# Optimization experiments

Measured on AMD Instinct MI355X. Metric: run time of the kernel, lower is better.

The kernel has to match this reference:

```python
import jax, jax.numpy as jnp
import numpy as np

V, D, H, F = 50257, 180, 18, 720
S = 2048
DK = D // H  # 10
EPS = 1e-5


def _layernorm(x, g, b):
    mu = jnp.mean(x, axis=-1, keepdims=True)
    var = jnp.mean(jnp.square(x - mu), axis=-1, keepdims=True)
    return (x - mu) * jax.lax.rsqrt(var + EPS) * g + b


def _pos_encoding(seq_len, d_model):
    pos = jnp.arange(seq_len, dtype=jnp.float32)[:, None]            # [S,1]
    i = jnp.arange(d_model // 2, dtype=jnp.float32)[None, :]         # [1,D/2]
    angle = pos / jnp.power(10000.0, 2.0 * i / d_model)              # [S,D/2]
    pe = jnp.zeros((seq_len, d_model), dtype=jnp.float32)
    pe = pe.at[:, 0::2].set(jnp.sin(angle))
    pe = pe.at[:, 1::2].set(jnp.cos(angle))
    return pe


def setup_inputs() -> dict:
    key = jax.random.key(0)
    ks = jax.random.split(key, 16)

    def xavier(k, shape):
        fan_out, fan_in = shape[0], shape[-1]
        lim = float(np.sqrt(6.0 / (fan_in + fan_out)))
        return jax.random.uniform(k, shape, jnp.float32, -lim, lim)

    return {
        "input_ids": jax.random.randint(ks[0], (S,), 0, V),
        "emb": xavier(ks[1], (V, D)),
        "Wq": xavier(ks[2], (D, D)),
        "Wk": xavier(ks[3], (D, D)),
        "Wv": xavier(ks[4], (D, D)),
        "g1": jnp.ones((D,), jnp.float32),
        "beta1": jnp.zeros((D,), jnp.float32),
        "W1": xavier(ks[5], (F, D)),
        "bf1": jnp.zeros((F,), jnp.float32),
        "W2": xavier(ks[6], (D, F)),
        "bf2": jnp.zeros((D,), jnp.float32),
        "g2": jnp.ones((D,), jnp.float32),
        "beta2": jnp.zeros((D,), jnp.float32),
        "Wo": xavier(ks[7], (V, D)),
        "bo": jnp.zeros((V,), jnp.float32),
    }


def reference(input_ids, emb, Wq, Wk, Wv, g1, beta1, W1, bf1, W2, bf2, g2, beta2, Wo, bo):
    seq_len = input_ids.shape[0]
    x = emb[input_ids] + _pos_encoding(seq_len, D)                   # [S,D]

    # QKV projections (no bias), split into heads: [H,S,DK]
    q = (x @ Wq.T).reshape(seq_len, H, DK).transpose(1, 0, 2)
    k = (x @ Wk.T).reshape(seq_len, H, DK).transpose(1, 0, 2)
    v = (x @ Wv.T).reshape(seq_len, H, DK).transpose(1, 0, 2)

    scores = jnp.einsum("hqd,hkd->hqk", q, k) / jnp.sqrt(jnp.float32(DK))
    causal = jnp.tril(jnp.ones((seq_len, seq_len), dtype=bool))
    scores = jnp.where(causal[None, :, :], scores, -1e9)
    attn = jax.nn.softmax(scores, axis=-1)
    out = jnp.einsum("hqk,hkd->hqd", attn, v)                        # [H,S,DK]
    attn_out = out.transpose(1, 0, 2).reshape(seq_len, D)

    x = _layernorm(x + attn_out, g1, beta1)
    ff = jax.nn.gelu(x @ W1.T + bf1, approximate=False) @ W2.T + bf2
    x = _layernorm(x + ff, g2, beta2)

    logits = x @ Wo.T + bo                                           # [S,V]
    return logits
```

## Files before the change

### kernel.cpp

```cpp
#include <hip/hip_runtime.h>
#include <hip/hip_bf16.h>

#define S 2048
#define D 180
#define H 18
#define DKH 10
#define F 720
#define V 50257
#define VP 51200
#define KP 192
#define EPS 1e-5f
#define NEGINF (-1e30f)

typedef __attribute__((ext_vector_type(8))) short bf16x8;
typedef __attribute__((ext_vector_type(4))) float f32x4;

__global__ void k_wbconv(const float* __restrict__ Wo, __hip_bfloat16* __restrict__ wb) {
    int idx = blockIdx.x * 256 + threadIdx.x;
    const int total = VP * 24;
    if (idx >= total) return;
    int n = idx / 24;
    int k0 = (idx - n * 24) * 8;
    __hip_bfloat16 tmp[8];
    #pragma unroll
    for (int j = 0; j < 8; ++j) {
        int k = k0 + j;
        float v = (n < V && k < D) ? Wo[n * D + k] : 0.0f;
        tmp[j] = __float2bfloat16(v);
    }
    *(bf16x8*)((short*)wb + n * KP + k0) = *(bf16x8*)tmp;
}

__global__ void k_transposeAll(const float* __restrict__ Wq, const float* __restrict__ Wk,
                               const float* __restrict__ Wv, const float* __restrict__ W1,
                               const float* __restrict__ W2,
                               float* __restrict__ WqT, float* __restrict__ WkT,
                               float* __restrict__ WvT, float* __restrict__ W1T,
                               float* __restrict__ W2T) {
    __shared__ float tile[32][33];
    const float* src; float* dst; int R, C;
    switch (blockIdx.y) {
        case 0: src = Wq; dst = WqT; R = D; C = D; break;
        case 1: src = Wk; dst = WkT; R = D; C = D; break;
        case 2: src = Wv; dst = WvT; R = D; C = D; break;
        case 3: src = W1; dst = W1T; R = F; C = D; break;
        default: src = W2; dst = W2T; R = D; C = F; break;
    }
    int tilesC = (C + 31) >> 5;
    int tr = (blockIdx.x / tilesC) * 32, tc = (blockIdx.x % tilesC) * 32;
    if (tr >= R) return;
    int lx = threadIdx.x & 31, ly = threadIdx.x >> 5;
    #pragma unroll
    for (int rr = ly; rr < 32; rr += 8) {
        int r = tr + rr, c = tc + lx;
        tile[rr][lx] = (r < R && c < C) ? src[r * C + c] : 0.0f;
    }
    __syncthreads();
    #pragma unroll
    for (int rr = ly; rr < 32; rr += 8) {
        int c = tc + rr, r = tr + lx;
        if (c < C && r < R) dst[c * R + r] = tile[lx][rr];
    }
}

__global__ void k_qkv(const int* __restrict__ ids, const float* __restrict__ emb,
                      const float* __restrict__ WqT, const float* __restrict__ WkT,
                      const float* __restrict__ WvT,
                      float* __restrict__ x0, float* __restrict__ qkv) {
    const int R = 8;
    __shared__ float xs[R * D];
    int r0 = blockIdx.x * R;
    const float* WT = (blockIdx.y == 0) ? WqT : ((blockIdx.y == 1) ? WkT : WvT);
    float* out = qkv + blockIdx.y * (S * D);
    for (int idx = threadIdx.x; idx < R * D; idx += 192) {
        int r = idx / D, d = idx - r * D;
        int row = r0 + r;
        int i = d >> 1;
        float inv = exp2f(-0.14764124866166054f * (float)i);
        float ang = (float)row * inv;
        float pe = (d & 1) ? cosf(ang) : sinf(ang);
        float v = emb[(size_t)ids[row] * D + d] + pe;
        xs[idx] = v;
        if (blockIdx.y == 0) x0[(size_t)row * D + d] = v;
    }
    __syncthreads();
    int d = threadIdx.x;
    if (d < D) {
        float acc[R] = {};
        for (int k0 = 0; k0 < D; k0 += 4) {
            f32x4 xr[R];
            #pragma unroll
            for (int r = 0; r < R; ++r) xr[r] = *(const f32x4*)&xs[r * D + k0];
            #pragma unroll
            for (int j = 0; j < 4; ++j) {
                float wv = WT[(k0 + j) * D + d];
                #pragma unroll
                for (int r = 0; r < R; ++r) acc[r] += xr[r][j] * wv;
            }
        }
        #pragma unroll
        for (int r = 0; r < R; ++r) out[(r0 + r) * D + d] = acc[r];
    }
}

__global__ __launch_bounds__(256) void k_attn1(const float* __restrict__ qkv,
                                               float* __restrict__ part) {
    int c = blockIdx.x, qt = blockIdx.y, h = blockIdx.z;
    if (4 * c > qt) return;
    __shared__ float Ks[256][12];
    __shared__ float Vs[256][12];
    __shared__ float cmb[4][64][13];
    int j0 = c * 256, q0 = qt * 64;
    int t = threadIdx.x;
    int lane = t & 63, w = t >> 6;
    const float* kp = qkv + S * D + h * DKH;
    const float* vp = qkv + 2 * S * D + h * DKH;
    for (int e = t; e < 256 * DKH; e += 256) {
        int jj = e / DKH, cc = e - jj * DKH;
        Ks[jj][cc] = kp[(j0 + jj) * D + cc];
        Vs[jj][cc] = vp[(j0 + jj) * D + cc];
    }
    __syncthreads();
    int qi = q0 + lane;
    float qv[DKH];
    #pragma unroll
    for (int cc = 0; cc < DKH; ++cc) qv[cc] = qkv[qi * D + h * DKH + cc];
    float m = NEGINF, l = 0.0f, acc[DKH] = {};
    const float scale = 0.31622776601683794f;
    #pragma unroll
    for (int blk = 0; blk < 8; ++blk) {
        float sv[8], tm = NEGINF;
        #pragma unroll
        for (int u = 0; u < 8; ++u) {
            int jj = w * 64 + blk * 8 + u;
            int j = j0 + jj;
            f32x4 k0 = *(const f32x4*)&Ks[jj][0];
            f32x4 k1 = *(const f32x4*)&Ks[jj][4];
            f32x4 k2 = *(const f32x4*)&Ks[jj][8];
            float s = qv[0]*k0[0] + qv[1]*k0[1] + qv[2]*k0[2] + qv[3]*k0[3]
                    + qv[4]*k1[0] + qv[5]*k1[1] + qv[6]*k1[2] + qv[7]*k1[3]
                    + qv[8]*k2[0] + qv[9]*k2[1];
            sv[u] = (j <= qi) ? s * scale : NEGINF;
            tm = fmaxf(tm, sv[u]);
        }
        float nm = fmaxf(m, tm);
        if (nm > -0.5e30f) {
            float cor = __expf(m - nm);
            l *= cor;
            #pragma unroll
            for (int cc = 0; cc < DKH; ++cc) acc[cc] *= cor;
            m = nm;
            #pragma unroll
            for (int u = 0; u < 8; ++u) {
                float p = __expf(sv[u] - m);
                int jj = w * 64 + blk * 8 + u;
                l += p;
                f32x4 v0 = *(const f32x4*)&Vs[jj][0];
                f32x4 v1 = *(const f32x4*)&Vs[jj][4];
                f32x4 v2 = *(const f32x4*)&Vs[jj][8];
                acc[0] += p * v0[0]; acc[1] += p * v0[1];
                acc[2] += p * v0[2]; acc[3] += p * v0[3];
                acc[4] += p * v1[0]; acc[5] += p * v1[1];
                acc[6] += p * v1[2]; acc[7] += p * v1[3];
                acc[8] += p * v2[0]; acc[9] += p * v2[1];
            }
        }
    }
    cmb[w][lane][0] = m;
    cmb[w][lane][1] = l;
    #pragma unroll
    for (int cc = 0; cc < DKH; ++cc) cmb[w][lane][2 + cc] = acc[cc];
    __syncthreads();
    if (t < 64) {
        float M = NEGINF;
        #pragma unroll
        for (int ww = 0; ww < 4; ++ww) M = fmaxf(M, cmb[ww][t][0]);
        float L = 0.0f, o[DKH] = {};
        #pragma unroll
        for (int ww = 0; ww < 4; ++ww) {
            float e = __expf(cmb[ww][t][0] - M);
            L += e * cmb[ww][t][1];
            #pragma unroll
            for (int cc = 0; cc < DKH; ++cc) o[cc] += e * cmb[ww][t][2 + cc];
        }
        float* pp = part + (((size_t)(h * 32 + qt) * 9 + c) * 64 + t) * 12;
        pp[0] = M; pp[1] = L;
        #pragma unroll
        for (int cc = 0; cc < DKH; ++cc) pp[2 + cc] = o[cc];
    }
}

__global__ void k_attn2(const float* __restrict__ part, float* __restrict__ ao) {
    int qt = blockIdx.x, h = blockIdx.y;
    int q = threadIdx.x;
    int nch = qt / 4 + 1;
    float m = NEGINF, l = 0.0f, acc[DKH] = {};
    for (int c = 0; c < nch; ++c) {
        const float* pp = part + (((size_t)(h * 32 + qt) * 9 + c) * 64 + q) * 12;
        float pm = pp[0], pl = pp[1];
        float nm = fmaxf(m, pm);
        float c1 = __expf(m - nm), c2 = __expf(pm - nm);
        l = l * c1 + pl * c2;
        #pragma unroll
        for (int cc = 0; cc < DKH; ++cc)
            acc[cc] = acc[cc] * c1 + pp[2 + cc] * c2;
        m = nm;
    }
    float inv = 1.0f / l;
    float* op = ao + (size_t)(qt * 64 + q) * D + h * DKH;
    #pragma unroll
    for (int cc = 0; cc < DKH; ++cc) op[cc] = acc[cc] * inv;
}

__device__ inline float wave_sum(float v) {
    #pragma unroll
    for (int o = 32; o > 0; o >>= 1) v += __shfl_xor(v, o);
    return v;
}

__global__ void k_ln1(const float* __restrict__ x0, const float* __restrict__ ao,
                      const float* __restrict__ g, const float* __restrict__ b,
                      float* __restrict__ x1) {
    int row = blockIdx.x * 4 + (threadIdx.x >> 6);
    int lane = threadIdx.x & 63;
    const float* pa = x0 + row * D;
    const float* pb = ao + row * D;
    float v[3];
    int c[3];
    float sum = 0.0f;
    #pragma unroll
    for (int k = 0; k < 3; ++k) {
        c[k] = lane + 64 * k;
        v[k] = (c[k] < D) ? (pa[c[k]] + pb[c[k]]) : 0.0f;
        sum += v[k];
    }
    sum = wave_sum(sum);
    float mu = sum / (float)D;
    float ss = 0.0f;
    #pragma unroll
    for (int k = 0; k < 3; ++k) {
        float dd = (c[k] < D) ? (v[k] - mu) : 0.0f;
        ss += dd * dd;
    }
    ss = wave_sum(ss);
    float rs = rsqrtf(ss / (float)D + EPS);
    #pragma unroll
    for (int k = 0; k < 3; ++k)
        if (c[k] < D) x1[row * D + c[k]] = (v[k] - mu) * rs * g[c[k]] + b[c[k]];
}

__global__ __launch_bounds__(768) void k_ffn(const float* __restrict__ x1,
                     const float* __restrict__ W1T, const float* __restrict__ bf1,
                     const float* __restrict__ W2T, const float* __restrict__ bf2,
                     const float* __restrict__ g, const float* __restrict__ b,
                     __hip_bfloat16* __restrict__ xb) {
    const int R = 8;
    __shared__ float xs[R * D];
    __shared__ float ys[R * F];
    __shared__ float red[2][4][3][2];
    int r0 = blockIdx.x * R;
    int t = threadIdx.x;
    for (int idx = t; idx < R * D / 4; idx += 768)
        *(f32x4*)&xs[idx * 4] = *(const f32x4*)&x1[(size_t)r0 * D + idx * 4];
    __syncthreads();
    if (t < F) {
        float acc[R] = {};
        for (int k0 = 0; k0 < D; k0 += 4) {
            f32x4 xr[R];
            #pragma unroll
            for (int r = 0; r < R; ++r) xr[r] = *(const f32x4*)&xs[r * D + k0];
            #pragma unroll
            for (int j = 0; j < 4; ++j) {
                float wv = W1T[(k0 + j) * F + t];
                #pragma unroll
                for (int r = 0; r < R; ++r) acc[r] += xr[r][j] * wv;
            }
        }
        float bb = bf1[t];
        #pragma unroll
        for (int r = 0; r < R; ++r) {
            float vv = acc[r] + bb;
            ys[r * F + t] = 0.5f * vv * (1.0f + erff(vv * 0.7071067811865475f));
        }
    }
    __syncthreads();
    int gq = t / 192;
    int d = t - gq * 192;
    int wig = d >> 6;
    int lane = d & 63;
    int row0 = gq * 2, row1 = gq * 2 + 1;
    float v0 = 0.0f, v1 = 0.0f;
    if (d < D) {
        float a0 = 0.0f, a1 = 0.0f;
        for (int k0 = 0; k0 < F; k0 += 4) {
            f32x4 ya = *(const f32x4*)&ys[row0 * F + k0];
            f32x4 yb = *(const f32x4*)&ys[row1 * F + k0];
            #pragma unroll
            for (int j = 0; j < 4; ++j) {
                float wv = W2T[(k0 + j) * D + d];
                a0 += ya[j] * wv;
                a1 += yb[j] * wv;
            }
        }
        float bb = bf2[d];
        v0 = x1[(size_t)(r0 + row0) * D + d] + a0 + bb;
        v1 = x1[(size_t)(r0 + row1) * D + d] + a1 + bb;
    }
    {
        float s1 = wave_sum(v0), q1 = wave_sum(v0 * v0);
        float s2 = wave_sum(v1), q2 = wave_sum(v1 * v1);
        if (lane == 0) {
            red[0][gq][wig][0] = s1; red[1][gq][wig][0] = q1;
            red[0][gq][wig][1] = s2; red[1][gq][wig][1] = q2;
        }
    }
    __syncthreads();
    float sum0 = red[0][gq][0][0] + red[0][gq][1][0] + red[0][gq][2][0];
    float sq0  = red[1][gq][0][0] + red[1][gq][1][0] + red[1][gq][2][0];
    float sum1 = red[0][gq][0][1] + red[0][gq][1][1] + red[0][gq][2][1];
    float sq1  = red[1][gq][0][1] + red[1][gq][1][1] + red[1][gq][2][1];
    float mu0 = sum0 / (float)D, var0 = sq0 / (float)D - mu0 * mu0;
    float mu1 = sum1 / (float)D, var1 = sq1 / (float)D - mu1 * mu1;
    float rs0 = rsqrtf(var0 + EPS), rs1 = rsqrtf(var1 + EPS);
    float gd = (d < D) ? g[d] : 0.0f, bd = (d < D) ? b[d] : 0.0f;
    float o0 = (d < D) ? ((v0 - mu0) * rs0 * gd + bd) : 0.0f;
    float o1 = (d < D) ? ((v1 - mu1) * rs1 * gd + bd) : 0.0f;
    xb[(size_t)(r0 + row0) * KP + d] = __float2bfloat16(o0);
    xb[(size_t)(r0 + row1) * KP + d] = __float2bfloat16(o1);
}

__global__ __launch_bounds__(1024) void k_logits(const __hip_bfloat16* __restrict__ xbp,
                         const __hip_bfloat16* __restrict__ wbp,
                         const float* __restrict__ bo, float* __restrict__ out) {
    __shared__ float stg[16][16][68];
    int Lb = blockIdx.x;
    int wg = (Lb & 7) * 200 + (Lb >> 3);
    int mblk = wg & 31;
    int pblk = wg >> 5;
    int m0 = mblk * 64, n0 = pblk * 1024;
    int t = threadIdx.x;
    int lane = t & 63, wid = t >> 6;
    int r16 = lane & 15, kg = lane >> 4;
    int colbase = n0 + wid * 64;
    const short* xs = (const short*)xbp;
    const short* ws = (const short*)wbp;
    f32x4 acc[4][4] = {};
    int mrow[4], nrow[4];
    #pragma unroll
    for (int mi = 0; mi < 4; ++mi) mrow[mi] = m0 + mi * 16 + r16;
    #pragma unroll
    for (int ni = 0; ni < 4; ++ni) nrow[ni] = colbase + ni * 16 + r16;
    bf16x8 a0[4], b0[4];
    #pragma unroll
    for (int mi = 0; mi < 4; ++mi) a0[mi] = *(const bf16x8*)(xs + mrow[mi] * KP + kg * 8);
    #pragma unroll
    for (int ni = 0; ni < 4; ++ni) b0[ni] = *(const bf16x8*)(ws + nrow[ni] * KP + kg * 8);
    #pragma unroll
    for (int kk = 0; kk < 6; ++kk) {
        bf16x8 a1[4], b1[4];
        if (kk < 5) {
            int kb = (kk + 1) * 32 + kg * 8;
            #pragma unroll
            for (int mi = 0; mi < 4; ++mi) a1[mi] = *(const bf16x8*)(xs + mrow[mi] * KP + kb);
            #pragma unroll
            for (int ni = 0; ni < 4; ++ni) b1[ni] = *(const bf16x8*)(ws + nrow[ni] * KP + kb);
        }
        #pragma unroll
        for (int mi = 0; mi < 4; ++mi)
            #pragma unroll
            for (int ni = 0; ni < 4; ++ni)
                acc[mi][ni] = __builtin_amdgcn_mfma_f32_16x16x32_bf16(b0[ni], a0[mi], acc[mi][ni], 0, 0, 0);
        if (kk < 5) {
            #pragma unroll
            for (int mi = 0; mi < 4; ++mi) a0[mi] = a1[mi];
            #pragma unroll
            for (int ni = 0; ni < 4; ++ni) b0[ni] = b1[ni];
        }
    }
    bool ok = (colbase + lane < V);
    #pragma unroll
    for (int mi = 0; mi < 4; ++mi) {
        #pragma unroll
        for (int ni = 0; ni < 4; ++ni) {
            int cn = colbase + ni * 16 + kg * 4;
            f32x4 r = acc[mi][ni];
            if (cn + 3 < V) {
                f32x4 bv = *(const f32x4*)(bo + cn);
                r += bv;
            } else {
                #pragma unroll
                for (int j = 0; j < 4; ++j) r[j] += (cn + j < V) ? bo[cn + j] : 0.0f;
            }
            *(f32x4*)&stg[wid][r16][ni * 16 + kg * 4] = r;
        }
        float vals[16];
        #pragma unroll
        for (int rr = 0; rr < 16; ++rr) vals[rr] = stg[wid][rr][lane];
        float* p = out + (size_t)(m0 + mi * 16) * V + colbase + lane;
        #pragma unroll
        for (int rr = 0; rr < 16; ++rr) {
            if (ok) *p = vals[rr];
            p += V;
        }
    }
}

extern "C" void kernel_launch(void* const* d_in, const int* in_sizes, int n_in,
                              void* d_out, int out_size, void* d_ws, size_t ws_size,
                              hipStream_t stream) {
    const int* ids   = (const int*)d_in[0];
    const float* emb = (const float*)d_in[1];
    const float* Wq  = (const float*)d_in[2];
    const float* Wk  = (const float*)d_in[3];
    const float* Wv  = (const float*)d_in[4];
    const float* g1  = (const float*)d_in[5];
    const float* b1  = (const float*)d_in[6];
    const float* W1  = (const float*)d_in[7];
    const float* bf1 = (const float*)d_in[8];
    const float* W2  = (const float*)d_in[9];
    const float* bf2 = (const float*)d_in[10];
    const float* g2  = (const float*)d_in[11];
    const float* b2  = (const float*)d_in[12];
    const float* Wo  = (const float*)d_in[13];
    const float* bo  = (const float*)d_in[14];
    float* out = (float*)d_out;

    char* w = (char*)d_ws;
    float* x0 = (float*)w;           w += S * D * 4;
    float* qkv = (float*)w;          w += 3 * S * D * 4;
    float* ao = (float*)w;           w += S * D * 4;
    float* x1 = (float*)w;           w += S * D * 4;
    float* WqT = (float*)w;          w += D * D * 4;
    float* WkT = (float*)w;          w += D * D * 4;
    float* WvT = (float*)w;          w += D * D * 4;
    float* W1T = (float*)w;          w += F * D * 4;
    float* W2T = (float*)w;          w += D * F * 4;
    float* part = (float*)w;         w += (size_t)H * 32 * 9 * 64 * 12 * 4;
    __hip_bfloat16* xb = (__hip_bfloat16*)w; w += S * KP * 2;
    __hip_bfloat16* wb = (__hip_bfloat16*)w; w += (size_t)VP * KP * 2;

    k_wbconv<<<dim3((VP * 24 + 255) / 256), 256, 0, stream>>>(Wo, wb);
    k_transposeAll<<<dim3(138, 5), 256, 0, stream>>>(Wq, Wk, Wv, W1, W2,
                                                     WqT, WkT, WvT, W1T, W2T);
    k_qkv<<<dim3(S / 8, 3), 192, 0, stream>>>(ids, emb, WqT, WkT, WvT, x0, qkv);
    k_attn1<<<dim3(9, 32, H), 256, 0, stream>>>(qkv, part);
    k_attn2<<<dim3(32, H), 64, 0, stream>>>(part, ao);
    k_ln1<<<dim3(S / 4), 256, 0, stream>>>(x0, ao, g1, b1, x1);
    k_ffn<<<dim3(S / 8), 768, 0, stream>>>(x1, W1T, bf1, W2T, bf2, g2, b2, xb);
    k_logits<<<dim3(1600), 1024, 0, stream>>>(xb, wb, bo, out);
}
```

Baseline: 413.8 us.

## Split logits GEMM into tiled bf16 store plus separate relayout pass

The logits GEMM now writes bias-added results as bf16 into a tile-contiguous workspace buffer instead of staging them through shared memory into the strided fp32 output. A separate grid-stride kernel then reads those tiles and expands them to fp32 rows of the final output. The aim is to drop the LDS staging and make the GEMM's stores contiguous. The cost is an extra intermediate write and read, plus logits rounded to bf16 precision. The old direct kernel is kept as a fallback when the workspace is too small.

```diff
diff --git a/kernel.cpp b/kernel.cpp
--- a/kernel.cpp
+++ b/kernel.cpp
@@ -13,6 +13,7 @@
 #define NEGINF (-1e30f)
 
 typedef __attribute__((ext_vector_type(8))) short bf16x8;
+typedef __attribute__((ext_vector_type(4))) short short4v;
 typedef __attribute__((ext_vector_type(4))) float f32x4;
 
 __global__ void k_wbconv(const float* __restrict__ Wo, __hip_bfloat16* __restrict__ wb) {
@@ -329,7 +330,101 @@
     xb[(size_t)(r0 + row1) * KP + d] = __float2bfloat16(o1);
 }
 
-__global__ __launch_bounds__(1024) void k_logits(const __hip_bfloat16* __restrict__ xbp,
+__global__ __launch_bounds__(1024) void k_logits_g(const __hip_bfloat16* __restrict__ xbp,
+                         const __hip_bfloat16* __restrict__ wbp,
+                         const float* __restrict__ bo, short* __restrict__ lgt) {
+    int Lb = blockIdx.x;
+    int wg = (Lb & 7) * 200 + (Lb >> 3);
+    int mblk = wg & 31;
+    int pblk = wg >> 5;
+    int m0 = mblk * 64, n0 = pblk * 1024;
+    int t = threadIdx.x;
+    int lane = t & 63, wid = t >> 6;
+    int r16 = lane & 15, kg = lane >> 4;
+    int colbase = n0 + wid * 64;
+    const short* xs = (const short*)xbp;
+    const short* ws = (const short*)wbp;
+    f32x4 acc[4][4] = {};
+    int mrow[4], nrow[4];
+    #pragma unroll
+    for (int mi = 0; mi < 4; ++mi) mrow[mi] = m0 + mi * 16 + r16;
+    #pragma unroll
+    for (int ni = 0; ni < 4; ++ni) nrow[ni] = colbase + ni * 16 + r16;
+    bf16x8 a0[4], b0[4];
+    #pragma unroll
+    for (int mi = 0; mi < 4; ++mi) a0[mi] = *(const bf16x8*)(xs + mrow[mi] * KP + kg * 8);
+    #pragma unroll
+    for (int ni = 0; ni < 4; ++ni) b0[ni] = *(const bf16x8*)(ws + nrow[ni] * KP + kg * 8);
+    #pragma unroll
+    for (int kk = 0; kk < 6; ++kk) {
+        bf16x8 a1[4], b1[4];
+        if (kk < 5) {
+            int kb = (kk + 1) * 32 + kg * 8;
+            #pragma unroll
+            for (int mi = 0; mi < 4; ++mi) a1[mi] = *(const bf16x8*)(xs + mrow[mi] * KP + kb);
+            #pragma unroll
+            for (int ni = 0; ni < 4; ++ni) b1[ni] = *(const bf16x8*)(ws + nrow[ni] * KP + kb);
+        }
+        #pragma unroll
+        for (int mi = 0; mi < 4; ++mi)
+            #pragma unroll
+            for (int ni = 0; ni < 4; ++ni)
+                acc[mi][ni] = __builtin_amdgcn_mfma_f32_16x16x32_bf16(b0[ni], a0[mi], acc[mi][ni], 0, 0, 0);
+        if (kk < 5) {
+            #pragma unroll
+            for (int mi = 0; mi < 4; ++mi) a0[mi] = a1[mi];
+            #pragma unroll
+            for (int ni = 0; ni < 4; ++ni) b0[ni] = b1[ni];
+        }
+    }
+    short* dst = lgt + ((size_t)(mblk * 50 + pblk) << 16);
+    #pragma unroll
+    for (int mi = 0; mi < 4; ++mi) {
+        #pragma unroll
+        for (int ni = 0; ni < 4; ++ni) {
+            int cn = colbase + ni * 16 + kg * 4;
+            f32x4 r = acc[mi][ni];
+            if (cn + 3 < V) {
+                f32x4 bv = *(const f32x4*)(bo + cn);
+                r += bv;
+            } else {
+                #pragma unroll
+                for (int j = 0; j < 4; ++j) r[j] += (cn + j < V) ? bo[cn + j] : 0.0f;
+            }
+            short4v h;
+            #pragma unroll
+            for (int j = 0; j < 4; ++j)
+                h[j] = (short)__hip_bfloat16_raw(__float2bfloat16(r[j])).x;
+            int off = (mi * 16 + r16) * 1024 + wid * 64 + ni * 16 + kg * 4;
+            *(short4v*)(dst + off) = h;
+        }
+    }
+}
+
+#define C4PR 12565
+__global__ void k_relayout(const short* __restrict__ lgt, float* __restrict__ out) {
+    const unsigned total = (unsigned)S * C4PR;
+    for (unsigned w = blockIdx.x * 256 + threadIdx.x; w < total; w += gridDim.x * 256) {
+        unsigned row = w / C4PR;
+        unsigned c4 = w - row * C4PR;
+        unsigned col = c4 * 4;
+        unsigned tc = col >> 10, wc = col & 1023;
+        const short* p = lgt + (((size_t)((row >> 6) * 50 + tc)) << 16)
+                       + (row & 63) * 1024 + wc;
+        short4v h = *(const short4v*)p;
+        float* po = out + (size_t)row * V + col;
+        int n = V - col; n = (n > 4) ? 4 : n;
+        #pragma unroll
+        for (int j = 0; j < 4; ++j) {
+            if (j < n) {
+                unsigned u = ((unsigned)(unsigned short)h[j]) << 16;
+                po[j] = __uint_as_float(u);
+            }
+        }
+    }
+}
+
+__global__ __launch_bounds__(1024) void k_logits_direct(const __hip_bfloat16* __restrict__ xbp,
                          const __hip_bfloat16* __restrict__ wbp,
                          const float* __restrict__ bo, float* __restrict__ out) {
     __shared__ float stg[16][16][68];
@@ -438,6 +533,8 @@
     float* part = (float*)w;         w += (size_t)H * 32 * 9 * 64 * 12 * 4;
     __hip_bfloat16* xb = (__hip_bfloat16*)w; w += S * KP * 2;
     __hip_bfloat16* wb = (__hip_bfloat16*)w; w += (size_t)VP * KP * 2;
+    short* lgt = (short*)w;
+    size_t need = (size_t)(w - (char*)d_ws) + (size_t)S * VP * 2;
 
     k_wbconv<<<dim3((VP * 24 + 255) / 256), 256, 0, stream>>>(Wo, wb);
     k_transposeAll<<<dim3(138, 5), 256, 0, stream>>>(Wq, Wk, Wv, W1, W2,
@@ -447,5 +544,10 @@
     k_attn2<<<dim3(32, H), 64, 0, stream>>>(part, ao);
     k_ln1<<<dim3(S / 4), 256, 0, stream>>>(x0, ao, g1, b1, x1);
     k_ffn<<<dim3(S / 8), 768, 0, stream>>>(x1, W1T, bf1, W2T, bf2, g2, b2, xb);
-    k_logits<<<dim3(1600), 1024, 0, stream>>>(xb, wb, bo, out);
-}
+    if (ws_size >= need) {
+        k_logits_g<<<dim3(1600), 1024, 0, stream>>>(xb, wb, bo, lgt);
+        k_relayout<<<dim3(2048), 256, 0, stream>>>(lgt, out);
+    } else {
+        k_logits_direct<<<dim3(1600), 1024, 0, stream>>>(xb, wb, bo, out);
+    }
+}
```

Result: slower. 611.2 us (+47.7%).

## Restructure logits GEMM into LDS-staged 128x128 tiles with 2x2 wave layout

Applied to the files above, without the earlier changes.

Replaces the logits kernel, which read A and B fragments directly from global memory with 1024-thread blocks, with a 256-thread, 128x128-tile kernel. Each block stages A and B chunks of 64 K-elements into padded shared memory, prefetching the next chunk into registers while computing on the current one. The aim is to cut redundant global reads through reuse inside shared memory. The output epilogue now writes four scalar floats per lane directly instead of transposing through shared memory. That drops the coalesced store path for the 400MB output and may make the store-bound part worse.

```diff
diff --git a/kernel.cpp b/kernel.cpp
--- a/kernel.cpp
+++ b/kernel.cpp
@@ -11,6 +11,7 @@
 #define KP 192
 #define EPS 1e-5f
 #define NEGINF (-1e30f)
+#define LSTR 72
 
 typedef __attribute__((ext_vector_type(8))) short bf16x8;
 typedef __attribute__((ext_vector_type(4))) float f32x4;
@@ -329,80 +330,110 @@
     xb[(size_t)(r0 + row1) * KP + d] = __float2bfloat16(o1);
 }
 
-__global__ __launch_bounds__(1024) void k_logits(const __hip_bfloat16* __restrict__ xbp,
+__global__ __launch_bounds__(256) void k_logits(const __hip_bfloat16* __restrict__ xbp,
                          const __hip_bfloat16* __restrict__ wbp,
                          const float* __restrict__ bo, float* __restrict__ out) {
-    __shared__ float stg[16][16][68];
+    __shared__ short As[128 * LSTR];
+    __shared__ short Bs[128 * LSTR];
     int Lb = blockIdx.x;
-    int wg = (Lb & 7) * 200 + (Lb >> 3);
-    int mblk = wg & 31;
-    int pblk = wg >> 5;
-    int m0 = mblk * 64, n0 = pblk * 1024;
+    int wg = (Lb & 7) * 800 + (Lb >> 3);
+    int mblk = wg & 15;
+    int pblk = wg >> 4;
+    int m0 = mblk * 128, n0 = pblk * 128;
     int t = threadIdx.x;
     int lane = t & 63, wid = t >> 6;
+    int wy = wid >> 1, wx = wid & 1;
     int r16 = lane & 15, kg = lane >> 4;
-    int colbase = n0 + wid * 64;
     const short* xs = (const short*)xbp;
     const short* ws = (const short*)wbp;
+
+    int lrow = lane >> 3;
+    int lu = lane & 7;
+
+    bf16x8 ga[4], gb[4];
+    #define GLOAD(c)                                                              \
+    {                                                                             \
+        _Pragma("unroll")                                                         \
+        for (int tt = 0; tt < 4; ++tt) {                                          \
+            int row = wid * 32 + tt * 8 + lrow;                                   \
+            ga[tt] = *(const bf16x8*)(xs + (size_t)(m0 + row) * KP + (c) * 64 + lu * 8); \
+            gb[tt] = *(const bf16x8*)(ws + (size_t)(n0 + row) * KP + (c) * 64 + lu * 8); \
+        }                                                                         \
+    }
+    #define DSW()                                                                 \
+    {                                                                             \
+        _Pragma("unroll")                                                         \
+        for (int tt = 0; tt < 4; ++tt) {                                          \
+            int row = wid * 32 + tt * 8 + lrow;                                   \
+            *(bf16x8*)&As[row * LSTR + lu * 8] = ga[tt];                          \
+            *(bf16x8*)&Bs[row * LSTR + lu * 8] = gb[tt];                          \
+        }                                                                         \
+    }
+
     f32x4 acc[4][4] = {};
-    int mrow[4], nrow[4];
-    #pragma unroll
-    for (int mi = 0; mi < 4; ++mi) mrow[mi] = m0 + mi * 16 + r16;
-    #pragma unroll
-    for (int ni = 0; ni < 4; ++ni) nrow[ni] = colbase + ni * 16 + r16;
-    bf16x8 a0[4], b0[4];
-    #pragma unroll
-    for (int mi = 0; mi < 4; ++mi) a0[mi] = *(const bf16x8*)(xs + mrow[mi] * KP + kg * 8);
-    #pragma unroll
-    for (int ni = 0; ni < 4; ++ni) b0[ni] = *(const bf16x8*)(ws + nrow[ni] * KP + kg * 8);
-    #pragma unroll
-    for (int kk = 0; kk < 6; ++kk) {
-        bf16x8 a1[4], b1[4];
-        if (kk < 5) {
-            int kb = (kk + 1) * 32 + kg * 8;
-            #pragma unroll
-            for (int mi = 0; mi < 4; ++mi) a1[mi] = *(const bf16x8*)(xs + mrow[mi] * KP + kb);
-            #pragma unroll
-            for (int ni = 0; ni < 4; ++ni) b1[ni] = *(const bf16x8*)(ws + nrow[ni] * KP + kb);
-        }
-        #pragma unroll
-        for (int mi = 0; mi < 4; ++mi)
-            #pragma unroll
-            for (int ni = 0; ni < 4; ++ni)
-                acc[mi][ni] = __builtin_amdgcn_mfma_f32_16x16x32_bf16(b0[ni], a0[mi], acc[mi][ni], 0, 0, 0);
-        if (kk < 5) {
-            #pragma unroll
-            for (int mi = 0; mi < 4; ++mi) a0[mi] = a1[mi];
-            #pragma unroll
-            for (int ni = 0; ni < 4; ++ni) b0[ni] = b1[ni];
-        }
-    }
-    bool ok = (colbase + lane < V);
+    int arow[4], brow[4];
+    #pragma unroll
+    for (int mi = 0; mi < 4; ++mi) arow[mi] = wy * 64 + mi * 16 + r16;
+    #pragma unroll
+    for (int ni = 0; ni < 4; ++ni) brow[ni] = wx * 64 + ni * 16 + r16;
+
+    #define COMPUTE()                                                             \
+    {                                                                             \
+        _Pragma("unroll")                                                         \
+        for (int s = 0; s < 2; ++s) {                                             \
+            bf16x8 af[4], bfr[4];                                                 \
+            _Pragma("unroll")                                                     \
+            for (int mi = 0; mi < 4; ++mi)                                        \
+                af[mi] = *(const bf16x8*)&As[arow[mi] * LSTR + (s * 4 + kg) * 8]; \
+            _Pragma("unroll")                                                     \
+            for (int ni = 0; ni < 4; ++ni)                                        \
+                bfr[ni] = *(const bf16x8*)&Bs[brow[ni] * LSTR + (s * 4 + kg) * 8];\
+            _Pragma("unroll")                                                     \
+            for (int mi = 0; mi < 4; ++mi)                                        \
+                _Pragma("unroll")                                                 \
+                for (int ni = 0; ni < 4; ++ni)                                    \
+                    acc[mi][ni] = __builtin_amdgcn_mfma_f32_16x16x32_bf16(        \
+                        bfr[ni], af[mi], acc[mi][ni], 0, 0, 0);                   \
+        }                                                                         \
+    }
+
+    GLOAD(0)
+    DSW()
+    __syncthreads();
+    GLOAD(1)
+    COMPUTE()
+    __syncthreads();
+    DSW()
+    __syncthreads();
+    GLOAD(2)
+    COMPUTE()
+    __syncthreads();
+    DSW()
+    __syncthreads();
+    COMPUTE()
+
     #pragma unroll
     for (int mi = 0; mi < 4; ++mi) {
+        int row = m0 + wy * 64 + mi * 16 + r16;
+        float* orow = out + (size_t)row * V;
         #pragma unroll
         for (int ni = 0; ni < 4; ++ni) {
-            int cn = colbase + ni * 16 + kg * 4;
+            int cn = n0 + wx * 64 + ni * 16 + kg * 4;
             f32x4 r = acc[mi][ni];
             if (cn + 3 < V) {
-                f32x4 bv = *(const f32x4*)(bo + cn);
-                r += bv;
+                r += *(const f32x4*)(bo + cn);
+                orow[cn] = r[0]; orow[cn + 1] = r[1];
+                orow[cn + 2] = r[2]; orow[cn + 3] = r[3];
             } else {
                 #pragma unroll
-                for (int j = 0; j < 4; ++j) r[j] += (cn + j < V) ? bo[cn + j] : 0.0f;
+                for (int j = 0; j < 4; ++j)
+                    if (cn + j < V) orow[cn + j] = r[j] + bo[cn + j];
             }
-            *(f32x4*)&stg[wid][r16][ni * 16 + kg * 4] = r;
-        }
-        float vals[16];
-        #pragma unroll
-        for (int rr = 0; rr < 16; ++rr) vals[rr] = stg[wid][rr][lane];
-        float* p = out + (size_t)(m0 + mi * 16) * V + colbase + lane;
-        #pragma unroll
-        for (int rr = 0; rr < 16; ++rr) {
-            if (ok) *p = vals[rr];
-            p += V;
-        }
-    }
+        }
+    }
+    #undef GLOAD
+    #undef DSW
+    #undef COMPUTE
 }
 
 extern "C" void kernel_launch(void* const* d_in, const int* in_sizes, int n_in,
@@ -447,5 +478,5 @@
     k_attn2<<<dim3(32, H), 64, 0, stream>>>(part, ao);
     k_ln1<<<dim3(S / 4), 256, 0, stream>>>(x0, ao, g1, b1, x1);
     k_ffn<<<dim3(S / 8), 768, 0, stream>>>(x1, W1T, bf1, W2T, bf2, g2, b2, xb);
-    k_logits<<<dim3(1600), 1024, 0, stream>>>(xb, wb, bo, out);
-}
+    k_logits<<<dim3(6400), 256, 0, stream>>>(xb, wb, bo, out);
+}
```

New measurement: 350.4 us. 1.18x faster.
